# Performance work log

Measured on AMD Instinct MI355X. Metric: run time of the kernel, lower is better.

Reference implementation:

```python
import jax, jax.numpy as jnp
import numpy as np

VOCAB, E, H, HOPS, HEADS = 32000, 128, 256, 3, 4
N, TM, WLEN, TQ = 32, 50, 20, 20


def _gru(x_tbe, h0, Wih, Whh, bih, bhh):
    # x_tbe: [T, B, E] time-major; h0: [B, H]. PyTorch GRU gate order (r, z, n).
    def step(h, xt):
        gi = xt @ Wih.T + bih
        gh = h @ Whh.T + bhh
        ir, iz, inn = jnp.split(gi, 3, axis=-1)
        hr, hz, hn = jnp.split(gh, 3, axis=-1)
        r = jax.nn.sigmoid(ir + hr)
        z = jax.nn.sigmoid(iz + hz)
        n = jnp.tanh(inn + r * hn)
        return (1.0 - z) * n + z * h, None
    h, _ = jax.lax.scan(step, h0, x_tbe)
    return h


def setup_inputs() -> dict:
    key = jax.random.key(0)
    ks = jax.random.split(key, 24)
    f32 = jnp.float32
    emb = jax.random.uniform(ks[0], (VOCAB, E), f32, -3 ** 0.5, 3 ** 0.5)
    emb = emb.at[0].set(0.0)  # padding_idx=0
    s = 0.05
    inp = {
        'stories': jax.random.randint(ks[1], (N, TM, WLEN), 0, VOCAB),
        'questions': jax.random.randint(ks[2], (N, TQ), 0, VOCAB),
        'emb': emb,
        'q_Wih': jax.random.normal(ks[3], (3 * H, E), f32) * s,
        'q_Whh': jax.random.normal(ks[4], (3 * H, H), f32) * s,
        'q_bih': jnp.zeros((3 * H,), f32),
        'q_bhh': jnp.zeros((3 * H,), f32),
        'i_Wih': jax.random.normal(ks[5], (3 * H, E), f32) * s,
        'i_Whh': jax.random.normal(ks[6], (3 * H, H), f32) * s,
        'i_bih': jnp.zeros((3 * H,), f32),
        'i_bhh': jnp.zeros((3 * H,), f32),
        'Wm': jax.random.normal(ks[7], (HOPS, HEADS, H, H), f32) * s,
        'Wo_w': jax.random.normal(ks[8], (HOPS, H, HEADS * H), f32) * s,
        'Wo_b': jnp.full((HOPS, H), 0.01, f32),
        'ft_W1': jax.random.normal(ks[9], (H, H), f32) * s,
        'ft_b1': jnp.full((H,), 0.01, f32),
        'ft_W2': jax.random.normal(ks[10], (H, H), f32) * s,
        'ft_b2': jnp.full((H,), 0.01, f32),
        'g_W1': jax.random.normal(ks[11], (3 * H, 3 * H), f32) * s,
        'g_b1': jnp.full((3 * H,), 0.01, f32),
        'g_W2': jax.random.normal(ks[12], (3 * H, 3 * H), f32) * s,
        'g_b2': jnp.full((3 * H,), 0.01, f32),
        'V_w': jax.random.normal(ks[13], (VOCAB, 3 * H), f32) * s,
    }
    return inp


def reference(stories, questions, emb, q_Wih, q_Whh, q_bih, q_bhh,
              i_Wih, i_Whh, i_bih, i_bhh, Wm, Wo_w, Wo_b,
              ft_W1, ft_b1, ft_W2, ft_b2, g_W1, g_b1, g_W2, g_b2, V_w):
    n, tm, _ = stories.shape
    h = i_Whh.shape[1]
    hops, heads = Wm.shape[0], Wm.shape[1]

    # ---- input module: per-batch-item GRU; hidden state carries across batch items (as in source loop) ----
    story_embs = emb[stories]  # [N, TM, W, E]
    def bstep(hid, se):  # se: [TM, W, E]
        hid2 = _gru(jnp.swapaxes(se, 0, 1), hid, i_Wih, i_Whh, i_bih, i_bhh)
        return hid2, hid2
    _, memory = jax.lax.scan(bstep, jnp.zeros((tm, h), emb.dtype), story_embs)  # [N, TM, H]

    # ---- question module ----
    q_emb = emb[questions]  # [N, TQ, E]
    q = _gru(jnp.swapaxes(q_emb, 0, 1), jnp.zeros((n, h), emb.dtype), q_Wih, q_Whh, q_bih, q_bhh)  # [N, H]

    def ft(x):
        return jax.nn.relu(jax.nn.relu(x @ ft_W1.T + ft_b1) @ ft_W2.T + ft_b2)

    # ---- multi-hop attention controllers ----
    o_k = ft(q)
    buffers = []
    for hp in range(hops):
        proj = jnp.tanh(jnp.einsum('ntd,hed->nhte', memory, Wm[hp]))      # [N,heads,TM,H]
        scores = jax.nn.softmax(jnp.einsum('nhte,ne->nht', proj, o_k), axis=-1)
        rep = jnp.einsum('nht,ntd->nhd', scores, memory)                   # [N,heads,H]
        buf = rep.reshape(n, heads * h) @ Wo_w[hp].T + Wo_b[hp]            # [N,H]
        buffers.append(buf)
        o_k = ft(buf)
    wb = jnp.stack(buffers, axis=1)  # [N, HOPS, H]

    # ---- RM: all-pairs relation MLP (dropout = identity in eval) ----
    npair = hops * hops
    left = jnp.broadcast_to(wb[:, None, :, :], (n, hops, hops, h)).reshape(n, npair, h)
    right = jnp.broadcast_to(wb[:, :, None, :], (n, hops, hops, h)).reshape(n, npair, h)
    qx = jnp.broadcast_to(q[:, None, :], (n, npair, h))
    comb = jnp.concatenate([left, right, qx], axis=-1)                     # [N, HOPS^2, 3H]
    g = jax.nn.relu(jax.nn.relu(comb @ g_W1.T + g_b1) @ g_W2.T + g_b2)
    reasoning = g.sum(axis=1)                                              # [N, 3H]
    return reasoning @ V_w.T                                               # [N, VOCAB]
```

## Files before the change

kernel.cpp:

```cpp
#include <hip/hip_runtime.h>
#include <cmath>

#define VOCABN 32000
#define EE 128
#define HH 256
#define H3 768
#define HOPSN 3
#define HEADSN 4
#define NB 32
#define TMN 50
#define WLENN 20
#define TQN 20
#define NPOS (NB*TMN*WLENN)
#define NQPOS (NB*TQN)

#define OFF_MEM    0
#define OFF_Q      (OFF_MEM + NB*TMN*HH)
#define OFF_OK     (OFF_Q + NB*HH)
#define OFF_WB     (OFF_OK + NB*HH)
#define OFF_REP    (OFF_WB + NB*HOPSN*HH)
#define OFF_REAS   (OFF_REP + NB*HEADSN*HH)
#define OFF_GI     (OFF_REAS + NB*H3)

typedef __fp16 h2 __attribute__((ext_vector_type(2)));

__device__ __forceinline__ float sigm(float x) { return 1.f / (1.f + expf(-x)); }

__device__ __forceinline__ unsigned packh2(float x, float y) {
    h2 h = __builtin_amdgcn_cvt_pkrtz(x, y);
    return __builtin_bit_cast(unsigned, h);
}

__device__ __forceinline__ float fdot2u(unsigned a, unsigned b, float c) {
    return __builtin_amdgcn_fdot2(__builtin_bit_cast(h2, a),
                                  __builtin_bit_cast(h2, b), c, false);
}

#define GIB 64
__global__ __launch_bounds__(768) void k_gi(const int* __restrict__ stories,
                                            const int* __restrict__ questions,
                                            const float* __restrict__ emb,
                                            const float* __restrict__ iWih,
                                            const float* __restrict__ qWih,
                                            const float* __restrict__ ibih, const float* __restrict__ ibhh,
                                            const float* __restrict__ qbih, const float* __restrict__ qbhh,
                                            float* __restrict__ ws)
{
    __shared__ unsigned xs[GIB][EE / 2];
    __fp16* __restrict__ gi = (__fp16*)(ws + OFF_GI);
    const int j = threadIdx.x;
    const bool isq = blockIdx.x >= (NPOS / GIB);
    const int pblk = isq ? (blockIdx.x - NPOS / GIB) : blockIdx.x;
    const int p0 = pblk * GIB;
    const size_t g0 = (isq ? (size_t)NPOS : 0) + (size_t)p0;
    const int* __restrict__ toks = isq ? (questions + p0) : (stories + p0);
    const float* __restrict__ Wih = isq ? qWih : iWih;
    const float* __restrict__ bih = isq ? qbih : ibih;
    const float* __restrict__ bhh = isq ? qbhh : ibhh;
    const float bias = (j < 2 * HH) ? (bih[j] + bhh[j]) : bih[j];
    unsigned wreg[EE / 2];
    const float2* wrow = reinterpret_cast<const float2*>(Wih + (size_t)j * EE);
    #pragma unroll
    for (int c = 0; c < EE / 2; ++c) {
        const float2 w2 = wrow[c];
        wreg[c] = packh2(w2.x, w2.y);
    }
    for (int idx = j; idx < GIB * (EE / 2); idx += H3) {
        const int p = idx >> 6, c = idx & 63;
        const int tok = toks[p];
        const float2 e2 = reinterpret_cast<const float2*>(emb + (size_t)tok * EE)[c];
        xs[p][c] = packh2(e2.x, e2.y);
    }
    __syncthreads();
    for (int p = 0; p < GIB; ++p) {
        float acc = bias;
        #pragma unroll
        for (int c = 0; c < EE / 2; ++c) acc = fdot2u(xs[p][c], wreg[c], acc);
        gi[(g0 + p) * H3 + j] = (__fp16)acc;
    }
}

__global__ __launch_bounds__(1024, 4) void k_gru4(
    const float* __restrict__ iWhh, const float* __restrict__ qWhh,
    const float* __restrict__ ibhh, const float* __restrict__ qbhh,
    float* __restrict__ ws)
{
    __shared__ unsigned hp32[HH / 2];
    __shared__ float red[HH * 13];
    const int tid = threadIdx.x;
    const int j = tid & 255, kq = tid >> 8;
    const int blk = blockIdx.x;
    const bool isq = blk >= TMN;
    const float* __restrict__ Whh = isq ? qWhh : iWhh;
    unsigned wg0[32], wg1[32], wg2[32];
    {
        const float2* r0 = reinterpret_cast<const float2*>(Whh + (size_t)j * HH + kq * 64);
        const float2* r1 = reinterpret_cast<const float2*>(Whh + (size_t)(HH + j) * HH + kq * 64);
        const float2* r2 = reinterpret_cast<const float2*>(Whh + (size_t)(2 * HH + j) * HH + kq * 64);
        #pragma unroll
        for (int c = 0; c < 32; ++c) { const float2 a = r0[c]; wg0[c] = packh2(a.x, a.y); }
        #pragma unroll
        for (int c = 0; c < 32; ++c) { const float2 a = r1[c]; wg1[c] = packh2(a.x, a.y); }
        #pragma unroll
        for (int c = 0; c < 32; ++c) { const float2 a = r2[c]; wg2[c] = packh2(a.x, a.y); }
    }
    float bnH = 0.f, hstate = 0.f;
    if (kq == 0) bnH = (isq ? qbhh : ibhh)[2 * HH + j];
    if (tid < HH / 2) hp32[tid] = 0u;
    const __fp16* __restrict__ gib = (const __fp16*)(ws + OFF_GI)
                                     + (isq ? (size_t)NPOS * H3 : 0);
    float* __restrict__ memv = ws + OFF_MEM;
    float* __restrict__ qv   = ws + OFF_Q;
    __syncthreads();

    const int nOuter = isq ? 1 : NB;
    const int c = isq ? (blk - TMN) : blk;
    for (int n = 0; n < nOuter; ++n) {
        for (int t = 0; t < WLENN; ++t) {
            const int pos = isq ? (c * TQN + t) : ((n * TMN + c) * WLENN + t);
            float gir = 0.f, giz = 0.f, gin = 0.f;
            if (kq == 0) {
                const size_t gb = (size_t)pos * H3;
                gir = (float)gib[gb + j];
                giz = (float)gib[gb + HH + j];
                gin = (float)gib[gb + 2 * HH + j];
            }
            float a0 = 0.f, a1 = 0.f, a2 = 0.f;
            const uint4* hp4 = reinterpret_cast<const uint4*>(hp32);
            #pragma unroll
            for (int c4 = 0; c4 < 8; ++c4) {
                const uint4 hh = hp4[kq * 8 + c4];
                a0 = fdot2u(hh.x, wg0[4 * c4 + 0], a0);
                a0 = fdot2u(hh.y, wg0[4 * c4 + 1], a0);
                a0 = fdot2u(hh.z, wg0[4 * c4 + 2], a0);
                a0 = fdot2u(hh.w, wg0[4 * c4 + 3], a0);
                a1 = fdot2u(hh.x, wg1[4 * c4 + 0], a1);
                a1 = fdot2u(hh.y, wg1[4 * c4 + 1], a1);
                a1 = fdot2u(hh.z, wg1[4 * c4 + 2], a1);
                a1 = fdot2u(hh.w, wg1[4 * c4 + 3], a1);
                a2 = fdot2u(hh.x, wg2[4 * c4 + 0], a2);
                a2 = fdot2u(hh.y, wg2[4 * c4 + 1], a2);
                a2 = fdot2u(hh.z, wg2[4 * c4 + 2], a2);
                a2 = fdot2u(hh.w, wg2[4 * c4 + 3], a2);
            }
            red[j * 13 + kq]     = a0;
            red[j * 13 + 4 + kq] = a1;
            red[j * 13 + 8 + kq] = a2;
            __syncthreads();
            if (kq == 0) {
                const float* rr = red + j * 13;
                const float s0 = (rr[0] + rr[1]) + (rr[2] + rr[3]);
                const float s1 = (rr[4] + rr[5]) + (rr[6] + rr[7]);
                const float s2 = (rr[8] + rr[9]) + (rr[10] + rr[11]);
                const float r  = sigm(s0 + gir);
                const float z  = sigm(s1 + giz);
                const float nn = tanhf(gin + r * (s2 + bnH));
                hstate = (1.f - z) * nn + z * hstate;
                reinterpret_cast<__fp16*>(hp32)[j] = (__fp16)hstate;
                if (t == WLENN - 1) {
                    if (isq) qv[c * HH + j] = hstate;
                    else     memv[(size_t)(n * TMN + c) * HH + j] = hstate;
                }
            }
            __syncthreads();
        }
    }
}

__global__ __launch_bounds__(256) void k_ft(const float* __restrict__ src, float* __restrict__ dst,
                                            const float* __restrict__ W1, const float* __restrict__ b1,
                                            const float* __restrict__ W2, const float* __restrict__ b2)
{
    __shared__ float xr[HH];
    __shared__ float y1[HH];
    const int n = blockIdx.x, j = threadIdx.x;
    xr[j] = src[n * HH + j];
    __syncthreads();
    float acc = b1[j];
    const float4* w1 = reinterpret_cast<const float4*>(W1 + j * HH);
    #pragma unroll 4
    for (int k4 = 0; k4 < HH / 4; ++k4) {
        const float4 w = w1[k4];
        const float4 x = *reinterpret_cast<const float4*>(&xr[k4 * 4]);
        acc = fmaf(x.x, w.x, fmaf(x.y, w.y, fmaf(x.z, w.z, fmaf(x.w, w.w, acc))));
    }
    y1[j] = fmaxf(acc, 0.f);
    __syncthreads();
    acc = b2[j];
    const float4* w2 = reinterpret_cast<const float4*>(W2 + j * HH);
    #pragma unroll 4
    for (int k4 = 0; k4 < HH / 4; ++k4) {
        const float4 w = w2[k4];
        const float4 x = *reinterpret_cast<const float4*>(&y1[k4 * 4]);
        acc = fmaf(x.x, w.x, fmaf(x.y, w.y, fmaf(x.z, w.z, fmaf(x.w, w.w, acc))));
    }
    dst[n * HH + j] = fmaxf(acc, 0.f);
}

__global__ __launch_bounds__(256) void k_attn(const float* __restrict__ Wm, float* __restrict__ ws, int hp)
{
    __shared__ float mem_s[TMN][HH];
    __shared__ float ok_s[HH];
    __shared__ float wred[4][TMN];
    __shared__ float sc[TMN];
    const int n = blockIdx.x / HEADSN, hh = blockIdx.x % HEADSN;
    const int e = threadIdx.x;
    const float* __restrict__ memory = ws + OFF_MEM + n * TMN * HH;
    for (int idx = e; idx < TMN * HH; idx += HH)
        (&mem_s[0][0])[idx] = memory[idx];
    ok_s[e] = (ws + OFF_OK)[n * HH + e];
    __syncthreads();

    float p[TMN];
    #pragma unroll
    for (int t = 0; t < TMN; ++t) p[t] = 0.f;
    const float4* wrow = reinterpret_cast<const float4*>(Wm + ((size_t)(hp * HEADSN + hh) * HH + e) * HH);
    for (int d4 = 0; d4 < HH / 4; ++d4) {
        const float4 w = wrow[d4];
        #pragma unroll
        for (int t = 0; t < TMN; ++t) {
            const float4 m = *reinterpret_cast<const float4*>(&mem_s[t][d4 * 4]);
            p[t] = fmaf(m.x, w.x, fmaf(m.y, w.y, fmaf(m.z, w.z, fmaf(m.w, w.w, p[t]))));
        }
    }
    const float okv = ok_s[e];
    const int lane = e & 63, wv = e >> 6;
    #pragma unroll
    for (int t = 0; t < TMN; ++t) {
        float v = tanhf(p[t]) * okv;
        #pragma unroll
        for (int off = 32; off > 0; off >>= 1) v += __shfl_xor(v, off);
        if (lane == 0) wred[wv][t] = v;
    }
    __syncthreads();
    if (e < TMN) sc[e] = wred[0][e] + wred[1][e] + wred[2][e] + wred[3][e];
    __syncthreads();
    if (e == 0) {
        float mx = sc[0];
        for (int t = 1; t < TMN; ++t) mx = fmaxf(mx, sc[t]);
        float sum = 0.f;
        for (int t = 0; t < TMN; ++t) { const float ex = expf(sc[t] - mx); sc[t] = ex; sum += ex; }
        const float inv = 1.f / sum;
        for (int t = 0; t < TMN; ++t) sc[t] *= inv;
    }
    __syncthreads();
    float r = 0.f;
    #pragma unroll
    for (int t = 0; t < TMN; ++t) r = fmaf(sc[t], mem_s[t][e], r);
    (ws + OFF_REP)[(n * HEADSN + hh) * HH + e] = r;
}

__global__ __launch_bounds__(256) void k_buf(const float* __restrict__ Wo_w, const float* __restrict__ Wo_b,
                                             const float* __restrict__ W1, const float* __restrict__ b1,
                                             const float* __restrict__ W2, const float* __restrict__ b2,
                                             float* __restrict__ ws, int hp)
{
    __shared__ float repf[HEADSN * HH];
    __shared__ float bufs[HH];
    __shared__ float y1[HH];
    const int n = blockIdx.x, j = threadIdx.x;
    const float* __restrict__ rep = ws + OFF_REP + n * HEADSN * HH;
    for (int idx = j; idx < HEADSN * HH; idx += HH) repf[idx] = rep[idx];
    __syncthreads();
    float acc = Wo_b[hp * HH + j];
    const float4* wrow = reinterpret_cast<const float4*>(Wo_w + ((size_t)hp * HH + j) * (HEADSN * HH));
    #pragma unroll 4
    for (int c4 = 0; c4 < HEADSN * HH / 4; ++c4) {
        const float4 w = wrow[c4];
        const float4 x = *reinterpret_cast<const float4*>(&repf[c4 * 4]);
        acc = fmaf(x.x, w.x, fmaf(x.y, w.y, fmaf(x.z, w.z, fmaf(x.w, w.w, acc))));
    }
    (ws + OFF_WB)[(n * HOPSN + hp) * HH + j] = acc;
    bufs[j] = acc;
    __syncthreads();
    float a1 = b1[j];
    const float4* w1 = reinterpret_cast<const float4*>(W1 + j * HH);
    #pragma unroll 4
    for (int k4 = 0; k4 < HH / 4; ++k4) {
        const float4 w = w1[k4];
        const float4 x = *reinterpret_cast<const float4*>(&bufs[k4 * 4]);
        a1 = fmaf(x.x, w.x, fmaf(x.y, w.y, fmaf(x.z, w.z, fmaf(x.w, w.w, a1))));
    }
    y1[j] = fmaxf(a1, 0.f);
    __syncthreads();
    float a2 = b2[j];
    const float4* w2 = reinterpret_cast<const float4*>(W2 + j * HH);
    #pragma unroll 4
    for (int k4 = 0; k4 < HH / 4; ++k4) {
        const float4 w = w2[k4];
        const float4 x = *reinterpret_cast<const float4*>(&y1[k4 * 4]);
        a2 = fmaf(x.x, w.x, fmaf(x.y, w.y, fmaf(x.z, w.z, fmaf(x.w, w.w, a2))));
    }
    (ws + OFF_OK)[n * HH + j] = fmaxf(a2, 0.f);
}

__global__ __launch_bounds__(768) void k_rm(const float* __restrict__ gW1, const float* __restrict__ gb1,
                                            const float* __restrict__ gW2, const float* __restrict__ gb2,
                                            float* __restrict__ ws)
{
    __shared__ float comb[9][H3];
    __shared__ float y1[9][H3];
    const int n = blockIdx.x;
    const int o = threadIdx.x;
    const float* __restrict__ wb = ws + OFF_WB + n * HOPSN * HH;
    const float* __restrict__ qv = ws + OFF_Q + n * HH;
    #pragma unroll
    for (int p = 0; p < 9; ++p) {
        const int ii = p / 3, jj = p % 3;
        float v;
        if (o < HH)            v = wb[jj * HH + o];
        else if (o < 2 * HH)   v = wb[ii * HH + (o - HH)];
        else                   v = qv[o - 2 * HH];
        comb[p][o] = v;
    }
    __syncthreads();
    float acc[9];
    #pragma unroll
    for (int p = 0; p < 9; ++p) acc[p] = gb1[o];
    const float4* w1 = reinterpret_cast<const float4*>(gW1 + (size_t)o * H3);
    for (int c4 = 0; c4 < H3 / 4; ++c4) {
        const float4 w = w1[c4];
        #pragma unroll
        for (int p = 0; p < 9; ++p) {
            const float4 x = *reinterpret_cast<const float4*>(&comb[p][c4 * 4]);
            acc[p] = fmaf(x.x, w.x, fmaf(x.y, w.y, fmaf(x.z, w.z, fmaf(x.w, w.w, acc[p]))));
        }
    }
    #pragma unroll
    for (int p = 0; p < 9; ++p) y1[p][o] = fmaxf(acc[p], 0.f);
    __syncthreads();
    #pragma unroll
    for (int p = 0; p < 9; ++p) acc[p] = gb2[o];
    const float4* w2 = reinterpret_cast<const float4*>(gW2 + (size_t)o * H3);
    for (int c4 = 0; c4 < H3 / 4; ++c4) {
        const float4 w = w2[c4];
        #pragma unroll
        for (int p = 0; p < 9; ++p) {
            const float4 x = *reinterpret_cast<const float4*>(&y1[p][c4 * 4]);
            acc[p] = fmaf(x.x, w.x, fmaf(x.y, w.y, fmaf(x.z, w.z, fmaf(x.w, w.w, acc[p]))));
        }
    }
    float s = 0.f;
    #pragma unroll
    for (int p = 0; p < 9; ++p) s += fmaxf(acc[p], 0.f);
    (ws + OFF_REAS)[n * H3 + o] = s;
}

__global__ __launch_bounds__(256) void k_out(const float* __restrict__ V_w, const float* __restrict__ ws,
                                             float* __restrict__ out)
{
    __shared__ float rs[NB * H3];
    const int v = blockIdx.x * 256 + threadIdx.x;
    for (int idx = threadIdx.x; idx < NB * H3; idx += 256) rs[idx] = (ws + OFF_REAS)[idx];
    __syncthreads();
    float acc[NB];
    #pragma unroll
    for (int nn = 0; nn < NB; ++nn) acc[nn] = 0.f;
    const float4* vw = reinterpret_cast<const float4*>(V_w + (size_t)v * H3);
    for (int d4 = 0; d4 < H3 / 4; ++d4) {
        const float4 w = vw[d4];
        #pragma unroll
        for (int nn = 0; nn < NB; ++nn) {
            const float4 r = *reinterpret_cast<const float4*>(&rs[nn * H3 + d4 * 4]);
            acc[nn] = fmaf(r.x, w.x, fmaf(r.y, w.y, fmaf(r.z, w.z, fmaf(r.w, w.w, acc[nn]))));
        }
    }
    #pragma unroll
    for (int nn = 0; nn < NB; ++nn) out[(size_t)nn * VOCABN + v] = acc[nn];
}

extern "C" void kernel_launch(void* const* d_in, const int* in_sizes, int n_in,
                              void* d_out, int out_size, void* d_ws, size_t ws_size,
                              hipStream_t stream)
{
    const int*   stories   = (const int*)d_in[0];
    const int*   questions = (const int*)d_in[1];
    const float* emb   = (const float*)d_in[2];
    const float* qWih  = (const float*)d_in[3];
    const float* qWhh  = (const float*)d_in[4];
    const float* qbih  = (const float*)d_in[5];
    const float* qbhh  = (const float*)d_in[6];
    const float* iWih  = (const float*)d_in[7];
    const float* iWhh  = (const float*)d_in[8];
    const float* ibih  = (const float*)d_in[9];
    const float* ibhh  = (const float*)d_in[10];
    const float* Wm    = (const float*)d_in[11];
    const float* Wo_w  = (const float*)d_in[12];
    const float* Wo_b  = (const float*)d_in[13];
    const float* ftW1  = (const float*)d_in[14];
    const float* ftb1  = (const float*)d_in[15];
    const float* ftW2  = (const float*)d_in[16];
    const float* ftb2  = (const float*)d_in[17];
    const float* gW1   = (const float*)d_in[18];
    const float* gb1   = (const float*)d_in[19];
    const float* gW2   = (const float*)d_in[20];
    const float* gb2   = (const float*)d_in[21];
    const float* V_w   = (const float*)d_in[22];
    float* ws  = (float*)d_ws;
    float* out = (float*)d_out;

    hipLaunchKernelGGL(k_gi, dim3((NPOS + NQPOS) / GIB), dim3(H3), 0, stream,
                       stories, questions, emb, iWih, qWih, ibih, ibhh, qbih, qbhh, ws);
    hipLaunchKernelGGL(k_gru4, dim3(TMN + NB), dim3(1024), 0, stream,
                       iWhh, qWhh, ibhh, qbhh, ws);
    hipLaunchKernelGGL(k_ft, dim3(NB), dim3(HH), 0, stream, ws + OFF_Q, ws + OFF_OK, ftW1, ftb1, ftW2, ftb2);
    for (int hp = 0; hp < HOPSN; ++hp) {
        hipLaunchKernelGGL(k_attn, dim3(NB * HEADSN), dim3(HH), 0, stream, Wm, ws, hp);
        hipLaunchKernelGGL(k_buf, dim3(NB), dim3(HH), 0, stream, Wo_w, Wo_b, ftW1, ftb1, ftW2, ftb2, ws, hp);
    }
    hipLaunchKernelGGL(k_rm, dim3(NB), dim3(H3), 0, stream, gW1, gb1, gW2, gb2, ws);
    hipLaunchKernelGGL(k_out, dim3(VOCABN / 256), dim3(256), 0, stream, V_w, ws, out);
}
```

Measured before the change: 1.615 ms.

## Rework GRU split, split relation MLP, transpose output GEMV reduction layout

The GRU recurrence kernel now splits the hidden-dimension reduction across 2 thread groups instead of 4, using 512-thread blocks that hold larger fp16 weight slices in registers and do less shared-memory reduction per step. The relation MLP is split into two kernels spread over 96 blocks, with the intermediate activations staged in workspace, so more CUs work on it. The vocabulary projection stores the reasoning vectors transposed and padded in shared memory and has each thread handle 16 batch rows over 128 vocab entries. This gives more blocks and broadcast-friendly LDS reads, at the cost of reading V_w twice. The gi kernel also vectorizes its LDS reads to uint4. The larger register arrays in the GRU risk lowering occupancy or causing spills.

```diff
diff --git a/kernel.cpp b/kernel.cpp
--- a/kernel.cpp
+++ b/kernel.cpp
@@ -20,7 +20,8 @@
 #define OFF_WB     (OFF_OK + NB*HH)
 #define OFF_REP    (OFF_WB + NB*HOPSN*HH)
 #define OFF_REAS   (OFF_REP + NB*HEADSN*HH)
-#define OFF_GI     (OFF_REAS + NB*H3)
+#define OFF_Y1     (OFF_REAS + NB*H3)
+#define OFF_GI     (OFF_Y1 + NB*9*H3)
 
 typedef __fp16 h2 __attribute__((ext_vector_type(2)));
 
@@ -73,39 +74,46 @@
     }
     __syncthreads();
     for (int p = 0; p < GIB; ++p) {
+        const uint4* x4 = reinterpret_cast<const uint4*>(&xs[p][0]);
         float acc = bias;
         #pragma unroll
-        for (int c = 0; c < EE / 2; ++c) acc = fdot2u(xs[p][c], wreg[c], acc);
+        for (int c4 = 0; c4 < 16; ++c4) {
+            const uint4 xv = x4[c4];
+            acc = fdot2u(xv.x, wreg[4 * c4 + 0], acc);
+            acc = fdot2u(xv.y, wreg[4 * c4 + 1], acc);
+            acc = fdot2u(xv.z, wreg[4 * c4 + 2], acc);
+            acc = fdot2u(xv.w, wreg[4 * c4 + 3], acc);
+        }
         gi[(g0 + p) * H3 + j] = (__fp16)acc;
     }
 }
 
-__global__ __launch_bounds__(1024, 4) void k_gru4(
+__global__ __launch_bounds__(512, 2) void k_gru5(
     const float* __restrict__ iWhh, const float* __restrict__ qWhh,
     const float* __restrict__ ibhh, const float* __restrict__ qbhh,
     float* __restrict__ ws)
 {
     __shared__ unsigned hp32[HH / 2];
-    __shared__ float red[HH * 13];
+    __shared__ float red[HH * 5];
     const int tid = threadIdx.x;
-    const int j = tid & 255, kq = tid >> 8;
+    const int j = tid & 255, kh = tid >> 8;
     const int blk = blockIdx.x;
     const bool isq = blk >= TMN;
     const float* __restrict__ Whh = isq ? qWhh : iWhh;
-    unsigned wg0[32], wg1[32], wg2[32];
+    unsigned wg0[64], wg1[64], wg2[64];
     {
-        const float2* r0 = reinterpret_cast<const float2*>(Whh + (size_t)j * HH + kq * 64);
-        const float2* r1 = reinterpret_cast<const float2*>(Whh + (size_t)(HH + j) * HH + kq * 64);
-        const float2* r2 = reinterpret_cast<const float2*>(Whh + (size_t)(2 * HH + j) * HH + kq * 64);
-        #pragma unroll
-        for (int c = 0; c < 32; ++c) { const float2 a = r0[c]; wg0[c] = packh2(a.x, a.y); }
-        #pragma unroll
-        for (int c = 0; c < 32; ++c) { const float2 a = r1[c]; wg1[c] = packh2(a.x, a.y); }
-        #pragma unroll
-        for (int c = 0; c < 32; ++c) { const float2 a = r2[c]; wg2[c] = packh2(a.x, a.y); }
+        const float2* r0 = reinterpret_cast<const float2*>(Whh + (size_t)j * HH + kh * 128);
+        const float2* r1 = reinterpret_cast<const float2*>(Whh + (size_t)(HH + j) * HH + kh * 128);
+        const float2* r2 = reinterpret_cast<const float2*>(Whh + (size_t)(2 * HH + j) * HH + kh * 128);
+        #pragma unroll
+        for (int c = 0; c < 64; ++c) { const float2 a = r0[c]; wg0[c] = packh2(a.x, a.y); }
+        #pragma unroll
+        for (int c = 0; c < 64; ++c) { const float2 a = r1[c]; wg1[c] = packh2(a.x, a.y); }
+        #pragma unroll
+        for (int c = 0; c < 64; ++c) { const float2 a = r2[c]; wg2[c] = packh2(a.x, a.y); }
     }
     float bnH = 0.f, hstate = 0.f;
-    if (kq == 0) bnH = (isq ? qbhh : ibhh)[2 * HH + j];
+    if (kh == 0) bnH = (isq ? qbhh : ibhh)[2 * HH + j];
     if (tid < HH / 2) hp32[tid] = 0u;
     const __fp16* __restrict__ gib = (const __fp16*)(ws + OFF_GI)
                                      + (isq ? (size_t)NPOS * H3 : 0);
@@ -119,7 +127,7 @@
         for (int t = 0; t < WLENN; ++t) {
             const int pos = isq ? (c * TQN + t) : ((n * TMN + c) * WLENN + t);
             float gir = 0.f, giz = 0.f, gin = 0.f;
-            if (kq == 0) {
+            if (kh == 0) {
                 const size_t gb = (size_t)pos * H3;
                 gir = (float)gib[gb + j];
                 giz = (float)gib[gb + HH + j];
@@ -128,8 +136,8 @@
             float a0 = 0.f, a1 = 0.f, a2 = 0.f;
             const uint4* hp4 = reinterpret_cast<const uint4*>(hp32);
             #pragma unroll
-            for (int c4 = 0; c4 < 8; ++c4) {
-                const uint4 hh = hp4[kq * 8 + c4];
+            for (int c4 = 0; c4 < 16; ++c4) {
+                const uint4 hh = hp4[kh * 16 + c4];
                 a0 = fdot2u(hh.x, wg0[4 * c4 + 0], a0);
                 a0 = fdot2u(hh.y, wg0[4 * c4 + 1], a0);
                 a0 = fdot2u(hh.z, wg0[4 * c4 + 2], a0);
@@ -143,18 +151,13 @@
                 a2 = fdot2u(hh.z, wg2[4 * c4 + 2], a2);
                 a2 = fdot2u(hh.w, wg2[4 * c4 + 3], a2);
             }
-            red[j * 13 + kq]     = a0;
-            red[j * 13 + 4 + kq] = a1;
-            red[j * 13 + 8 + kq] = a2;
+            if (kh == 1) { red[j * 5 + 0] = a0; red[j * 5 + 1] = a1; red[j * 5 + 2] = a2; }
             __syncthreads();
-            if (kq == 0) {
-                const float* rr = red + j * 13;
-                const float s0 = (rr[0] + rr[1]) + (rr[2] + rr[3]);
-                const float s1 = (rr[4] + rr[5]) + (rr[6] + rr[7]);
-                const float s2 = (rr[8] + rr[9]) + (rr[10] + rr[11]);
-                const float r  = sigm(s0 + gir);
-                const float z  = sigm(s1 + giz);
-                const float nn = tanhf(gin + r * (s2 + bnH));
+            if (kh == 0) {
+                const float* rr = red + j * 5;
+                const float r  = sigm(a0 + rr[0] + gir);
+                const float z  = sigm(a1 + rr[1] + giz);
+                const float nn = tanhf(gin + r * (a2 + rr[2] + bnH));
                 hstate = (1.f - z) * nn + z * hstate;
                 reinterpret_cast<__fp16*>(hp32)[j] = (__fp16)hstate;
                 if (t == WLENN - 1) {
@@ -294,49 +297,61 @@
     (ws + OFF_OK)[n * HH + j] = fmaxf(a2, 0.f);
 }
 
-__global__ __launch_bounds__(768) void k_rm(const float* __restrict__ gW1, const float* __restrict__ gb1,
-                                            const float* __restrict__ gW2, const float* __restrict__ gb2,
-                                            float* __restrict__ ws)
-{
-    __shared__ float comb[9][H3];
-    __shared__ float y1[9][H3];
-    const int n = blockIdx.x;
-    const int o = threadIdx.x;
+__global__ __launch_bounds__(256) void k_rm1(const float* __restrict__ gW1, const float* __restrict__ gb1,
+                                             float* __restrict__ ws)
+{
+    __shared__ float comb[9 * H3];
+    const int n = blockIdx.x / 3, ot = blockIdx.x % 3;
+    const int o = ot * 256 + threadIdx.x;
     const float* __restrict__ wb = ws + OFF_WB + n * HOPSN * HH;
     const float* __restrict__ qv = ws + OFF_Q + n * HH;
-    #pragma unroll
-    for (int p = 0; p < 9; ++p) {
+    for (int idx = threadIdx.x; idx < 9 * H3; idx += 256) {
+        const int p = idx / H3, cc = idx - p * H3;
         const int ii = p / 3, jj = p % 3;
         float v;
-        if (o < HH)            v = wb[jj * HH + o];
-        else if (o < 2 * HH)   v = wb[ii * HH + (o - HH)];
-        else                   v = qv[o - 2 * HH];
-        comb[p][o] = v;
+        if (cc < HH)           v = wb[jj * HH + cc];
+        else if (cc < 2 * HH)  v = wb[ii * HH + (cc - HH)];
+        else                   v = qv[cc - 2 * HH];
+        comb[idx] = v;
     }
     __syncthreads();
     float acc[9];
-    #pragma unroll
-    for (int p = 0; p < 9; ++p) acc[p] = gb1[o];
+    const float b = gb1[o];
+    #pragma unroll
+    for (int p = 0; p < 9; ++p) acc[p] = b;
     const float4* w1 = reinterpret_cast<const float4*>(gW1 + (size_t)o * H3);
     for (int c4 = 0; c4 < H3 / 4; ++c4) {
         const float4 w = w1[c4];
         #pragma unroll
         for (int p = 0; p < 9; ++p) {
-            const float4 x = *reinterpret_cast<const float4*>(&comb[p][c4 * 4]);
+            const float4 x = *reinterpret_cast<const float4*>(&comb[p * H3 + c4 * 4]);
             acc[p] = fmaf(x.x, w.x, fmaf(x.y, w.y, fmaf(x.z, w.z, fmaf(x.w, w.w, acc[p]))));
         }
     }
-    #pragma unroll
-    for (int p = 0; p < 9; ++p) y1[p][o] = fmaxf(acc[p], 0.f);
-    __syncthreads();
-    #pragma unroll
-    for (int p = 0; p < 9; ++p) acc[p] = gb2[o];
+    float* __restrict__ y1 = ws + OFF_Y1 + (size_t)n * 9 * H3;
+    #pragma unroll
+    for (int p = 0; p < 9; ++p) y1[p * H3 + o] = fmaxf(acc[p], 0.f);
+}
+
+__global__ __launch_bounds__(256) void k_rm2(const float* __restrict__ gW2, const float* __restrict__ gb2,
+                                             float* __restrict__ ws)
+{
+    __shared__ float y1s[9 * H3];
+    const int n = blockIdx.x / 3, ot = blockIdx.x % 3;
+    const int o = ot * 256 + threadIdx.x;
+    const float* __restrict__ y1 = ws + OFF_Y1 + (size_t)n * 9 * H3;
+    for (int idx = threadIdx.x; idx < 9 * H3; idx += 256) y1s[idx] = y1[idx];
+    __syncthreads();
+    float acc[9];
+    const float b = gb2[o];
+    #pragma unroll
+    for (int p = 0; p < 9; ++p) acc[p] = b;
     const float4* w2 = reinterpret_cast<const float4*>(gW2 + (size_t)o * H3);
     for (int c4 = 0; c4 < H3 / 4; ++c4) {
         const float4 w = w2[c4];
         #pragma unroll
         for (int p = 0; p < 9; ++p) {
-            const float4 x = *reinterpret_cast<const float4*>(&y1[p][c4 * 4]);
+            const float4 x = *reinterpret_cast<const float4*>(&y1s[p * H3 + c4 * 4]);
             acc[p] = fmaf(x.x, w.x, fmaf(x.y, w.y, fmaf(x.z, w.z, fmaf(x.w, w.w, acc[p]))));
         }
     }
@@ -346,27 +361,42 @@
     (ws + OFF_REAS)[n * H3 + o] = s;
 }
 
+#define RST 36
 __global__ __launch_bounds__(256) void k_out(const float* __restrict__ V_w, const float* __restrict__ ws,
                                              float* __restrict__ out)
 {
-    __shared__ float rs[NB * H3];
-    const int v = blockIdx.x * 256 + threadIdx.x;
-    for (int idx = threadIdx.x; idx < NB * H3; idx += 256) rs[idx] = (ws + OFF_REAS)[idx];
-    __syncthreads();
-    float acc[NB];
-    #pragma unroll
-    for (int nn = 0; nn < NB; ++nn) acc[nn] = 0.f;
+    __shared__ float rsT[H3 * RST];
+    const int tid = threadIdx.x;
+    const int v = blockIdx.x * 128 + (tid & 127);
+    const int nh = tid >> 7;
+    for (int idx = tid; idx < NB * H3; idx += 256) {
+        const int n = idx / H3, d = idx - n * H3;
+        rsT[d * RST + n] = (ws + OFF_REAS)[idx];
+    }
+    __syncthreads();
+    float acc[16];
+    #pragma unroll
+    for (int i = 0; i < 16; ++i) acc[i] = 0.f;
     const float4* vw = reinterpret_cast<const float4*>(V_w + (size_t)v * H3);
     for (int d4 = 0; d4 < H3 / 4; ++d4) {
         const float4 w = vw[d4];
         #pragma unroll
-        for (int nn = 0; nn < NB; ++nn) {
-            const float4 r = *reinterpret_cast<const float4*>(&rs[nn * H3 + d4 * 4]);
-            acc[nn] = fmaf(r.x, w.x, fmaf(r.y, w.y, fmaf(r.z, w.z, fmaf(r.w, w.w, acc[nn]))));
-        }
-    }
-    #pragma unroll
-    for (int nn = 0; nn < NB; ++nn) out[(size_t)nn * VOCABN + v] = acc[nn];
+        for (int dd = 0; dd < 4; ++dd) {
+            const float wd = (dd == 0) ? w.x : (dd == 1) ? w.y : (dd == 2) ? w.z : w.w;
+            const float* rr = &rsT[(d4 * 4 + dd) * RST + nh * 16];
+            #pragma unroll
+            for (int q = 0; q < 4; ++q) {
+                const float4 r4 = *reinterpret_cast<const float4*>(rr + 4 * q);
+                acc[4 * q + 0] = fmaf(wd, r4.x, acc[4 * q + 0]);
+                acc[4 * q + 1] = fmaf(wd, r4.y, acc[4 * q + 1]);
+                acc[4 * q + 2] = fmaf(wd, r4.z, acc[4 * q + 2]);
+                acc[4 * q + 3] = fmaf(wd, r4.w, acc[4 * q + 3]);
+            }
+        }
+    }
+    #pragma unroll
+    for (int i = 0; i < 16; ++i)
+        out[(size_t)(nh * 16 + i) * VOCABN + v] = acc[i];
 }
 
 extern "C" void kernel_launch(void* const* d_in, const int* in_sizes, int n_in,
@@ -401,13 +431,14 @@
 
     hipLaunchKernelGGL(k_gi, dim3((NPOS + NQPOS) / GIB), dim3(H3), 0, stream,
                        stories, questions, emb, iWih, qWih, ibih, ibhh, qbih, qbhh, ws);
-    hipLaunchKernelGGL(k_gru4, dim3(TMN + NB), dim3(1024), 0, stream,
+    hipLaunchKernelGGL(k_gru5, dim3(TMN + NB), dim3(512), 0, stream,
                        iWhh, qWhh, ibhh, qbhh, ws);
     hipLaunchKernelGGL(k_ft, dim3(NB), dim3(HH), 0, stream, ws + OFF_Q, ws + OFF_OK, ftW1, ftb1, ftW2, ftb2);
     for (int hp = 0; hp < HOPSN; ++hp) {
         hipLaunchKernelGGL(k_attn, dim3(NB * HEADSN), dim3(HH), 0, stream, Wm, ws, hp);
         hipLaunchKernelGGL(k_buf, dim3(NB), dim3(HH), 0, stream, Wo_w, Wo_b, ftW1, ftb1, ftW2, ftb2, ws, hp);
     }
-    hipLaunchKernelGGL(k_rm, dim3(NB), dim3(H3), 0, stream, gW1, gb1, gW2, gb2, ws);
-    hipLaunchKernelGGL(k_out, dim3(VOCABN / 256), dim3(256), 0, stream, V_w, ws, out);
-}
+    hipLaunchKernelGGL(k_rm1, dim3(NB * 3), dim3(256), 0, stream, gW1, gb1, ws);
+    hipLaunchKernelGGL(k_rm2, dim3(NB * 3), dim3(256), 0, stream, gW2, gb2, ws);
+    hipLaunchKernelGGL(k_out, dim3(VOCABN / 128), dim3(256), 0, stream, V_w, ws, out);
+}
```

New measurement: 1.481 ms. 1.09x faster.
